# Optimization experiments

Measured on AMD Instinct MI355X. Metric: run time of the kernel, lower is better.

## Reference

```python
import jax, jax.numpy as jnp
import numpy as np

RING_SIZES = list(range(3, 27, 2))  # 3,5,...,25 -> 12 rings; (1+12)*96 = 1248
BN_EPS = 1e-5


def _box_sum(x, k):
    """Sum over k x k window (k odd), 'same' zero padding. x: [B,C,H,W].
    O(1) per pixel via summed-area table instead of dense depthwise conv."""
    p = k // 2
    H, W = x.shape[2], x.shape[3]
    xp = jnp.pad(x, ((0, 0), (0, 0), (p, p), (p, p)))
    S = jnp.cumsum(jnp.cumsum(xp, axis=2), axis=3)
    S = jnp.pad(S, ((0, 0), (0, 0), (1, 0), (1, 0)))  # leading zero row/col
    return (S[:, :, k:k + H, k:k + W] - S[:, :, :H, k:k + W]
            - S[:, :, k:k + H, :W] + S[:, :, :H, :W])


def _ring_sum(x, k):
    """Depthwise conv with a k x k ring of ones == box(k) - box(k-2)."""
    inner = x if k == 3 else _box_sum(x, k - 2)
    return _box_sum(x, k) - inner


def _bn_eval(x, gamma, beta, mean, var):
    scale = gamma / jnp.sqrt(var + BN_EPS)
    return x * scale[None, :, None, None] + (beta - mean * scale)[None, :, None, None]


def _conv1x1(x, w, b):
    # x: [B,C,H,W], w: [O,C] -> [B,O,H,W]
    return jnp.einsum('bchw,oc->bohw', x, w) + b[None, :, None, None]


def setup_inputs() -> dict:
    key = jax.random.key(0)
    ks = jax.random.split(key, 13)
    B, C, H, W = 4, 96, 128, 128
    return {
        'x': jax.random.normal(ks[0], (B, C, H, W), jnp.float32),
        'bn1_gamma': jax.random.uniform(ks[1], (1248,), jnp.float32, 0.5, 1.5),
        'bn1_beta': jax.random.normal(ks[2], (1248,), jnp.float32) * 0.1,
        'bn1_mean': jax.random.normal(ks[3], (1248,), jnp.float32),
        'bn1_var': jax.random.uniform(ks[4], (1248,), jnp.float32, 0.5, 1.5),
        'conv1_w': jax.random.normal(ks[5], (512, 1248), jnp.float32) * (1.0 / np.sqrt(1248)),
        'conv1_b': jax.random.normal(ks[6], (512,), jnp.float32) * 0.01,
        'bn2_gamma': jax.random.uniform(ks[7], (512,), jnp.float32, 0.5, 1.5),
        'bn2_beta': jax.random.normal(ks[8], (512,), jnp.float32) * 0.1,
        'bn2_mean': jax.random.normal(ks[9], (512,), jnp.float32),
        'bn2_var': jax.random.uniform(ks[10], (512,), jnp.float32, 0.5, 1.5),
        'conv2_w': jax.random.normal(ks[11], (96, 512), jnp.float32) * (1.0 / np.sqrt(512)),
        'conv2_b': jax.random.normal(ks[12], (96,), jnp.float32) * 0.01,
    }


def reference(x, bn1_gamma, bn1_beta, bn1_mean, bn1_var, conv1_w, conv1_b,
              bn2_gamma, bn2_beta, bn2_mean, bn2_var, conv2_w, conv2_b):
    convs = [x] + [_ring_sum(x, k) for k in RING_SIZES]
    h = jnp.concatenate(convs, axis=1)  # [B, 1248, H, W]
    h = _bn_eval(h, bn1_gamma, bn1_beta, bn1_mean, bn1_var)
    h = jax.nn.relu(_conv1x1(h, conv1_w, conv1_b))
    h = _bn_eval(h, bn2_gamma, bn2_beta, bn2_mean, bn2_var)
    return _conv1x1(h, conv2_w, conv2_b)
```

## Files before the change

kernel.cpp:

```cpp
#include <hip/hip_runtime.h>
#include <hip/hip_bf16.h>
#include <cstdint>

typedef __attribute__((ext_vector_type(8))) short bf16x8;
typedef __attribute__((ext_vector_type(4))) float f32x4;

#define BN_EPS 1e-5f

__global__ __launch_bounds__(256) void prep1_kernel(
    const float* __restrict__ W1, const float* __restrict__ cb1,
    const float* __restrict__ g1, const float* __restrict__ be1,
    const float* __restrict__ mu1, const float* __restrict__ va1,
    __hip_bfloat16* __restrict__ V, float* __restrict__ b1e)
{
  int o = blockIdx.x;
  int t = threadIdx.x;
  const float* wrow = W1 + (size_t)o * 1248;
  float acc = 0.f;
  for (int i = t; i < 1248; i += 256) {
    float s = g1[i] * rsqrtf(va1[i] + BN_EPS);
    float w = wrow[i];
    acc += w * (be1[i] - mu1[i] * s);
    float g = w * s;
    float gn = 0.f;
    if (i < 1152) {
      float sn = g1[i + 96] * rsqrtf(va1[i + 96] + BN_EPS);
      gn = wrow[i + 96] * sn;
    }
    V[(size_t)o * 1248 + i] = __float2bfloat16(g - gn);
  }
  for (int d = 32; d > 0; d >>= 1) acc += __shfl_down(acc, d);
  __shared__ float red[4];
  int lane = t & 63, wv = t >> 6;
  if (lane == 0) red[wv] = acc;
  __syncthreads();
  if (t == 0) b1e[o] = cb1[o] + red[0] + red[1] + red[2] + red[3];
}

__global__ __launch_bounds__(256) void prep2_kernel(
    const float* __restrict__ W2, const float* __restrict__ cb2,
    const float* __restrict__ g2, const float* __restrict__ be2,
    const float* __restrict__ mu2, const float* __restrict__ va2,
    __hip_bfloat16* __restrict__ W2e, float* __restrict__ b2e)
{
  int o = blockIdx.x;
  int t = threadIdx.x;
  const float* wrow = W2 + (size_t)o * 512;
  float acc = 0.f;
  for (int j = t; j < 512; j += 256) {
    float s = g2[j] * rsqrtf(va2[j] + BN_EPS);
    float wv = wrow[j];
    acc += wv * (be2[j] - mu2[j] * s);
    W2e[(size_t)o * 512 + j] = __float2bfloat16(wv * s);
  }
  for (int d = 32; d > 0; d >>= 1) acc += __shfl_down(acc, d);
  __shared__ float red[4];
  int lane = t & 63, wv2 = t >> 6;
  if (lane == 0) red[wv2] = acc;
  __syncthreads();
  if (t == 0) b2e[o] = cb2[o] + red[0] + red[1] + red[2] + red[3];
}

__global__ __launch_bounds__(128) void sat_kernel(
    const float* __restrict__ x, float* __restrict__ SAT)
{
  int plane = blockIdx.x;
  const float* xp = x + (size_t)plane * 16384;
  __shared__ float tile[16384];
  int t = threadIdx.x;
  for (int i4 = t; i4 < 4096; i4 += 128) {
    int r = i4 >> 5;
    int g = i4 & 31;
    float4 v = *(const float4*)(xp + (size_t)r * 128 + g * 4);
    *(float4*)(tile + r * 128 + ((g ^ (r & 31)) << 2)) = v;
  }
  __syncthreads();
  {
    int r = t;
    float carry = 0.f;
    for (int g = 0; g < 32; ++g) {
      float* p = tile + r * 128 + ((g ^ (r & 31)) << 2);
      float4 v = *(float4*)p;
      float s0 = carry + v.x, s1 = s0 + v.y, s2 = s1 + v.z, s3 = s2 + v.w;
      float4 o; o.x = s0; o.y = s1; o.z = s2; o.w = s3;
      *(float4*)p = o;
      carry = s3;
    }
  }
  __syncthreads();
  float* Sg = SAT + (size_t)plane * 17028;
  Sg[t] = 0.f;
  if (t < 4) Sg[128 + t] = 0.f;
  Sg[(t + 1) * 132] = 0.f;
  int gc = t >> 2, wc = t & 3;
  float run = 0.f;
  for (int r = 0; r < 128; ++r) {
    run += tile[r * 128 + ((gc ^ (r & 31)) << 2) + wc];
    Sg[(r + 1) * 132 + t + 1] = run;
  }
}

__global__ __launch_bounds__(1024) void fused1_kernel(
    const float* __restrict__ SAT, const __hip_bfloat16* __restrict__ V,
    const float* __restrict__ b1e, const __hip_bfloat16* __restrict__ W2e,
    const float* __restrict__ b2e, float* __restrict__ out, int nb, int b0)
{
  extern __shared__ __align__(16) char smem[];
  float* E = (float*)smem;
  __hip_bfloat16* As = (__hip_bfloat16*)(smem + 50688);

  int blk = blockIdx.x;
  int rows_per_xcd = (nb * 128) >> 3;
  int r = (blk & 7) * rows_per_xcd + (blk >> 3);
  int bL = r >> 7, y = r & 127;

  int t = threadIdx.x;
  int lane = t & 63, wv = t >> 6;
  int wm = wv & 1, wn = wv >> 1;
  int lr = lane & 15, quad = lane >> 4;
  int px = t & 127;
  int bg = t >> 7;

  const float* Sb = SAT + (size_t)bL * 96 * 17028;

  f32x4 acc[4][4];
#pragma unroll
  for (int i = 0; i < 4; ++i)
#pragma unroll
    for (int jn = 0; jn < 4; ++jn) acc[i][jn] = (f32x4){0.f, 0.f, 0.f, 0.f};

  auto efill = [&](int j) {
    int y1 = (y - j < 0) ? 0 : (y - j);
    int y2 = ((y + j > 127) ? 127 : (y + j)) + 1;
    for (int idx = t; idx < 3168; idx += 1024) {
      int cl = idx / 33;
      int ck = idx - cl * 33;
      const float* bp = Sb + (size_t)cl * 17028 + ck * 4;
      float4 a = *(const float4*)(bp + y2 * 132);
      float4 b = *(const float4*)(bp + y1 * 132);
      float4 d;
      d.x = a.x - b.x; d.y = a.y - b.y; d.z = a.z - b.z; d.w = a.w - b.w;
      *(float4*)(E + cl * 132 + ck * 4) = d;
    }
  };

  efill(0);
  __syncthreads();

  for (int j = 0; j < 13; ++j) {
    int x1 = (px - j < 0) ? 0 : (px - j);
    int x2 = ((px + j > 127) ? 127 : (px + j)) + 1;
    {
      const float* Eb = E + bg * 8 * 132;
      union { bf16x8 v; __hip_bfloat16 h[8]; } pk;
#pragma unroll
      for (int i = 0; i < 8; ++i)
        pk.h[i] = __float2bfloat16(Eb[i * 132 + x2] - Eb[i * 132 + x1]);
      *(bf16x8*)(As + px * 104 + bg * 8) = pk.v;
      if (bg < 4) {
        const float* Eb2 = E + (8 + bg) * 8 * 132;
        union { bf16x8 v; __hip_bfloat16 h[8]; } pk2;
#pragma unroll
        for (int i = 0; i < 8; ++i)
          pk2.h[i] = __float2bfloat16(Eb2[i * 132 + x2] - Eb2[i * 132 + x1]);
        *(bf16x8*)(As + px * 104 + (8 + bg) * 8) = pk2.v;
      }
    }
    __syncthreads();

#pragma unroll
    for (int sub = 0; sub < 3; ++sub) {
      bf16x8 af[4], bfr[4];
#pragma unroll
      for (int i = 0; i < 4; ++i)
        af[i] = *(const bf16x8*)(As + (wm * 64 + i * 16 + lr) * 104 + sub * 32 + quad * 8);
#pragma unroll
      for (int jn = 0; jn < 4; ++jn)
        bfr[jn] = *(const bf16x8*)(V + (size_t)(wn * 64 + jn * 16 + lr) * 1248
                                   + j * 96 + sub * 32 + quad * 8);
#pragma unroll
      for (int i = 0; i < 4; ++i)
#pragma unroll
        for (int jn = 0; jn < 4; ++jn)
          acc[i][jn] = __builtin_amdgcn_mfma_f32_16x16x32_bf16(af[i], bfr[jn], acc[i][jn], 0, 0, 0);
      if (sub == 0 && j < 12) efill(j + 1);
    }
    __syncthreads();
  }

  __hip_bfloat16* Yst = (__hip_bfloat16*)smem;
#pragma unroll
  for (int jn = 0; jn < 4; ++jn) {
    int n = wn * 64 + jn * 16 + lr;
    float bias = b1e[n];
#pragma unroll
    for (int i = 0; i < 4; ++i) {
#pragma unroll
      for (int rr = 0; rr < 4; ++rr) {
        int m = wm * 64 + i * 16 + quad * 4 + rr;
        float z = acc[i][jn][rr] + bias;
        z = z > 0.f ? z : 0.f;
        Yst[m * 520 + n] = __float2bfloat16(z);
      }
    }
  }
  __syncthreads();

  int pxt = wv & 7;
  int mh = wv >> 3;
  f32x4 acc2[3];
#pragma unroll
  for (int im = 0; im < 3; ++im) acc2[im] = (f32x4){0.f, 0.f, 0.f, 0.f};

  for (int k2 = 0; k2 < 512; k2 += 32) {
    bf16x8 bfr2 = *(const bf16x8*)(Yst + (pxt * 16 + lr) * 520 + k2 + quad * 8);
#pragma unroll
    for (int im = 0; im < 3; ++im) {
      bf16x8 afr2 = *(const bf16x8*)(W2e + (size_t)(mh * 48 + im * 16 + lr) * 512
                                     + k2 + quad * 8);
      acc2[im] = __builtin_amdgcn_mfma_f32_16x16x32_bf16(afr2, bfr2, acc2[im], 0, 0, 0);
    }
  }

  size_t obase = ((size_t)(b0 + bL) * 96) * 16384 + (size_t)y * 128 + pxt * 16 + lr;
#pragma unroll
  for (int im = 0; im < 3; ++im) {
#pragma unroll
    for (int rr = 0; rr < 4; ++rr) {
      int o2 = mh * 48 + im * 16 + quad * 4 + rr;
      out[obase + (size_t)o2 * 16384] = acc2[im][rr] + b2e[o2];
    }
  }
}

extern "C" void kernel_launch(void* const* d_in, const int* in_sizes, int n_in,
                              void* d_out, int out_size, void* d_ws, size_t ws_size,
                              hipStream_t stream)
{
  const float* x   = (const float*)d_in[0];
  const float* g1  = (const float*)d_in[1];
  const float* be1 = (const float*)d_in[2];
  const float* mu1 = (const float*)d_in[3];
  const float* va1 = (const float*)d_in[4];
  const float* W1  = (const float*)d_in[5];
  const float* cb1 = (const float*)d_in[6];
  const float* g2  = (const float*)d_in[7];
  const float* be2 = (const float*)d_in[8];
  const float* mu2 = (const float*)d_in[9];
  const float* va2 = (const float*)d_in[10];
  const float* W2  = (const float*)d_in[11];
  const float* cb2 = (const float*)d_in[12];
  float* out = (float*)d_out;

  hipFuncSetAttribute((const void*)fused1_kernel,
                      hipFuncAttributeMaxDynamicSharedMemorySize, 133120);

  char* w = (char*)d_ws;
  __hip_bfloat16* V   = (__hip_bfloat16*)w; w += (size_t)512 * 1248 * 2;
  __hip_bfloat16* W2e = (__hip_bfloat16*)w; w += (size_t)96 * 512 * 2;
  float* b1e = (float*)w; w += 2048;
  float* b2e = (float*)w; w += 512;
  size_t fixed = (size_t)(w - (char*)d_ws);

  const size_t satB = (size_t)96 * 17028 * 4;
  int nb = (ws_size >= fixed + 4 * satB + 4096) ? 4 : 1;

  float* SAT = (float*)w;

  prep1_kernel<<<512, 256, 0, stream>>>(W1, cb1, g1, be1, mu1, va1, V, b1e);
  prep2_kernel<<<96, 256, 0, stream>>>(W2, cb2, g2, be2, mu2, va2, W2e, b2e);

  for (int b0 = 0; b0 < 4; b0 += nb) {
    sat_kernel<<<nb * 96, 128, 0, stream>>>(x + (size_t)b0 * 96 * 16384, SAT);
    fused1_kernel<<<nb * 128, 1024, 133120, stream>>>(SAT, V, b1e, W2e, b2e, out, nb, b0);
  }
}
```

Baseline: 302.2 us.

## Double-buffer E and A tiles in LDS and software-pipeline SAT loads two steps ahead

Double-buffers the row-difference buffer E and the bf16 A tile in shared memory. Global SAT loads for step j+2 are issued into registers before the MFMA work of step j and written back afterwards, and the A tile for j+1 is built after the MFMAs. This leaves one barrier per iteration instead of two and hides global latency behind the matrix work. In exchange it raises LDS use to about 151 KB and adds register pressure from holding 12 A and 12 B fragments plus the prefetched float4 values.

```diff
diff --git a/kernel.cpp b/kernel.cpp
--- a/kernel.cpp
+++ b/kernel.cpp
@@ -3,6 +3,7 @@
 #include <cstdint>
 
 typedef __attribute__((ext_vector_type(8))) short bf16x8;
+typedef __attribute__((ext_vector_type(4))) short bf16x4;
 typedef __attribute__((ext_vector_type(4))) float f32x4;
 
 #define BN_EPS 1e-5f
@@ -106,8 +107,10 @@
     const float* __restrict__ b2e, float* __restrict__ out, int nb, int b0)
 {
   extern __shared__ __align__(16) char smem[];
-  float* E = (float*)smem;
-  __hip_bfloat16* As = (__hip_bfloat16*)(smem + 50688);
+  const int EN = 96 * 132;
+  const int AN = 128 * 104;
+  float* E0 = (float*)smem;
+  __hip_bfloat16* A0 = (__hip_bfloat16*)(smem + 2 * EN * 4);
 
   int blk = blockIdx.x;
   int rows_per_xcd = (nb * 128) >> 3;
@@ -118,8 +121,7 @@
   int lane = t & 63, wv = t >> 6;
   int wm = wv & 1, wn = wv >> 1;
   int lr = lane & 15, quad = lane >> 4;
-  int px = t & 127;
-  int bg = t >> 7;
+  int pxb = t & 127;
 
   const float* Sb = SAT + (size_t)bL * 96 * 17028;
 
@@ -129,9 +131,10 @@
 #pragma unroll
     for (int jn = 0; jn < 4; ++jn) acc[i][jn] = (f32x4){0.f, 0.f, 0.f, 0.f};
 
-  auto efill = [&](int j) {
-    int y1 = (y - j < 0) ? 0 : (y - j);
-    int y2 = ((y + j > 127) ? 127 : (y + j)) + 1;
+  auto efill_now = [&](int jj) {
+    int y1 = (y - jj < 0) ? 0 : (y - jj);
+    int y2 = ((y + jj > 127) ? 127 : (y + jj)) + 1;
+    float* Ew = E0 + (jj & 1) * EN;
     for (int idx = t; idx < 3168; idx += 1024) {
       int cl = idx / 33;
       int ck = idx - cl * 33;
@@ -140,51 +143,106 @@
       float4 b = *(const float4*)(bp + y1 * 132);
       float4 d;
       d.x = a.x - b.x; d.y = a.y - b.y; d.z = a.z - b.z; d.w = a.w - b.w;
-      *(float4*)(E + cl * 132 + ck * 4) = d;
+      *(float4*)(Ew + cl * 132 + ck * 4) = d;
     }
   };
 
-  efill(0);
+  auto build = [&](int jj) {
+    const float* Eb = E0 + (jj & 1) * EN;
+    __hip_bfloat16* Ab = A0 + (jj & 1) * AN;
+    int x1 = (pxb - jj < 0) ? 0 : (pxb - jj);
+    int x2 = ((pxb + jj > 127) ? 127 : (pxb + jj)) + 1;
+#pragma unroll
+    for (int it = 0; it < 3; ++it) {
+      int hg = (t >> 7) + it * 8;
+      const float* Er = Eb + hg * 4 * 132;
+      union { bf16x4 v; __hip_bfloat16 h[4]; } pk;
+#pragma unroll
+      for (int i = 0; i < 4; ++i)
+        pk.h[i] = __float2bfloat16(Er[i * 132 + x2] - Er[i * 132 + x1]);
+      *(bf16x4*)(Ab + pxb * 104 + hg * 4) = pk.v;
+    }
+  };
+
+  efill_now(0);
+  __syncthreads();
+  build(0);
+  efill_now(1);
   __syncthreads();
 
   for (int j = 0; j < 13; ++j) {
-    int x1 = (px - j < 0) ? 0 : (px - j);
-    int x2 = ((px + j > 127) ? 127 : (px + j)) + 1;
+    float4 ea[4], eb[4];
+    int e_y1 = 0, e_y2 = 0;
+    bool do_e = (j < 11);
+    if (do_e) {
+      int jj = j + 2;
+      e_y1 = (y - jj < 0) ? 0 : (y - jj);
+      e_y2 = ((y + jj > 127) ? 127 : (y + jj)) + 1;
+#pragma unroll
+      for (int it = 0; it < 3; ++it) {
+        int idx = t + it * 1024;
+        int cl = idx / 33, ck = idx - cl * 33;
+        const float* bp = Sb + (size_t)cl * 17028 + ck * 4;
+        ea[it] = *(const float4*)(bp + e_y2 * 132);
+        eb[it] = *(const float4*)(bp + e_y1 * 132);
+      }
+      if (t < 96) {
+        int idx = t + 3072;
+        int cl = idx / 33, ck = idx - cl * 33;
+        const float* bp = Sb + (size_t)cl * 17028 + ck * 4;
+        ea[3] = *(const float4*)(bp + e_y2 * 132);
+        eb[3] = *(const float4*)(bp + e_y1 * 132);
+      }
+    }
+
     {
-      const float* Eb = E + bg * 8 * 132;
-      union { bf16x8 v; __hip_bfloat16 h[8]; } pk;
-#pragma unroll
-      for (int i = 0; i < 8; ++i)
-        pk.h[i] = __float2bfloat16(Eb[i * 132 + x2] - Eb[i * 132 + x1]);
-      *(bf16x8*)(As + px * 104 + bg * 8) = pk.v;
-      if (bg < 4) {
-        const float* Eb2 = E + (8 + bg) * 8 * 132;
-        union { bf16x8 v; __hip_bfloat16 h[8]; } pk2;
-#pragma unroll
-        for (int i = 0; i < 8; ++i)
-          pk2.h[i] = __float2bfloat16(Eb2[i * 132 + x2] - Eb2[i * 132 + x1]);
-        *(bf16x8*)(As + px * 104 + (8 + bg) * 8) = pk2.v;
-      }
-    }
-    __syncthreads();
-
-#pragma unroll
-    for (int sub = 0; sub < 3; ++sub) {
-      bf16x8 af[4], bfr[4];
-#pragma unroll
-      for (int i = 0; i < 4; ++i)
-        af[i] = *(const bf16x8*)(As + (wm * 64 + i * 16 + lr) * 104 + sub * 32 + quad * 8);
-#pragma unroll
-      for (int jn = 0; jn < 4; ++jn)
-        bfr[jn] = *(const bf16x8*)(V + (size_t)(wn * 64 + jn * 16 + lr) * 1248
-                                   + j * 96 + sub * 32 + quad * 8);
-#pragma unroll
-      for (int i = 0; i < 4; ++i)
+      const __hip_bfloat16* Aj = A0 + (j & 1) * AN;
+      bf16x8 af[12], bfr[12];
+#pragma unroll
+      for (int s = 0; s < 3; ++s)
+#pragma unroll
+        for (int i = 0; i < 4; ++i)
+          af[s * 4 + i] = *(const bf16x8*)(Aj + (wm * 64 + i * 16 + lr) * 104
+                                           + s * 32 + quad * 8);
+#pragma unroll
+      for (int s = 0; s < 3; ++s)
 #pragma unroll
         for (int jn = 0; jn < 4; ++jn)
-          acc[i][jn] = __builtin_amdgcn_mfma_f32_16x16x32_bf16(af[i], bfr[jn], acc[i][jn], 0, 0, 0);
-      if (sub == 0 && j < 12) efill(j + 1);
-    }
+          bfr[s * 4 + jn] = *(const bf16x8*)(V + (size_t)(wn * 64 + jn * 16 + lr) * 1248
+                                             + j * 96 + s * 32 + quad * 8);
+#pragma unroll
+      for (int s = 0; s < 3; ++s)
+#pragma unroll
+        for (int i = 0; i < 4; ++i)
+#pragma unroll
+          for (int jn = 0; jn < 4; ++jn)
+            acc[i][jn] = __builtin_amdgcn_mfma_f32_16x16x32_bf16(
+                af[s * 4 + i], bfr[s * 4 + jn], acc[i][jn], 0, 0, 0);
+    }
+
+    if (j < 12) build(j + 1);
+
+    if (do_e) {
+      float* Ew = E0 + (j & 1) * EN;
+#pragma unroll
+      for (int it = 0; it < 3; ++it) {
+        int idx = t + it * 1024;
+        int cl = idx / 33, ck = idx - cl * 33;
+        float4 d;
+        d.x = ea[it].x - eb[it].x; d.y = ea[it].y - eb[it].y;
+        d.z = ea[it].z - eb[it].z; d.w = ea[it].w - eb[it].w;
+        *(float4*)(Ew + cl * 132 + ck * 4) = d;
+      }
+      if (t < 96) {
+        int idx = t + 3072;
+        int cl = idx / 33, ck = idx - cl * 33;
+        float4 d;
+        d.x = ea[3].x - eb[3].x; d.y = ea[3].y - eb[3].y;
+        d.z = ea[3].z - eb[3].z; d.w = ea[3].w - eb[3].w;
+        *(float4*)(Ew + cl * 132 + ck * 4) = d;
+      }
+    }
+
     __syncthreads();
   }
 
@@ -253,7 +311,7 @@
   float* out = (float*)d_out;
 
   hipFuncSetAttribute((const void*)fused1_kernel,
-                      hipFuncAttributeMaxDynamicSharedMemorySize, 133120);
+                      hipFuncAttributeMaxDynamicSharedMemorySize, 154624);
 
   char* w = (char*)d_ws;
   __hip_bfloat16* V   = (__hip_bfloat16*)w; w += (size_t)512 * 1248 * 2;
@@ -272,6 +330,6 @@
 
   for (int b0 = 0; b0 < 4; b0 += nb) {
     sat_kernel<<<nb * 96, 128, 0, stream>>>(x + (size_t)b0 * 96 * 16384, SAT);
-    fused1_kernel<<<nb * 128, 1024, 133120, stream>>>(SAT, V, b1e, W2e, b2e, out, nb, b0);
-  }
-}
+    fused1_kernel<<<nb * 128, 1024, 154624, stream>>>(SAT, V, b1e, W2e, b2e, out, nb, b0);
+  }
+}
```

New measurement: 380.1 us. +25.8%, slower.
